# Kernel tuning notes

Measured on AMD Instinct MI355X. Metric: run time of the kernel, lower is better.

Reference implementation:

```python
import jax, jax.numpy as jnp
import numpy as np

K = 9            # LCN box-filter size
EPS = 1e-6


def _box_sum(x):
    """9x9 box sum with zero padding 4, separable. x: [N,H,W] -> [N,H,W]."""
    xp = x[:, None]                                  # N,1,H,W
    kh = jnp.ones((1, 1, K, 1), x.dtype)
    kw = jnp.ones((1, 1, 1, K), x.dtype)
    y = jax.lax.conv_general_dilated(xp, kh, (1, 1), [(K // 2, K // 2), (0, 0)])
    y = jax.lax.conv_general_dilated(y, kw, (1, 1), [(0, 0), (K // 2, K // 2)])
    return y[:, 0]


def _lcn(img):
    """Faithful to torch: conv weight is ones(3,3,9,9)/81, i.e. the 'mean' SUMS over
    the 3 input channels of per-pixel 9x9 box means; every output channel is identical.
    So compute channel-sum once, box-filter it, and broadcast back over channels."""
    kk = float(K * K)
    mean_local = _box_sum(img.sum(axis=1)) / kk                 # N,H,W
    mean_sq_local = _box_sum((img * img).sum(axis=1)) / kk      # N,H,W
    std_local = (mean_sq_local - mean_local * mean_local) * kk / (kk - 1.0)
    m = mean_local[:, None]                                     # N,1,H,W (broadcasts over C)
    s = std_local[:, None]
    return (img - m) / (s + EPS), m, s


def _warp(right, disp):
    """Equivalent of affine_grid(identity) + grid -= (disp*2/W, 0) + grid_sample
    (bilinear, zeros padding, align_corners=False). Since the y-coordinate is the
    identity grid, iy == row index exactly, so sampling reduces to 1-D horizontal
    bilinear interpolation at source column ix = j - disp[n,i,j]."""
    N, C, H, W = right.shape
    ix = jnp.arange(W, dtype=right.dtype)[None, None, :] - disp   # N,H,W
    x0 = jnp.floor(ix)
    wx = ix - x0                                                  # frac weight for x1
    x0i = x0.astype(jnp.int32)
    x1i = x0i + 1
    v0 = ((x0i >= 0) & (x0i < W)).astype(right.dtype)             # zeros padding masks
    v1 = ((x1i >= 0) & (x1i < W)).astype(right.dtype)
    i0 = jnp.broadcast_to(jnp.clip(x0i, 0, W - 1)[:, None], right.shape)
    i1 = jnp.broadcast_to(jnp.clip(x1i, 0, W - 1)[:, None], right.shape)
    g0 = jnp.take_along_axis(right, i0, axis=3)                   # N,C,H,W
    g1 = jnp.take_along_axis(right, i1, axis=3)
    return g0 * (v0 * (1.0 - wx))[:, None] + g1 * (v1 * wx)[:, None]


def setup_inputs() -> dict:
    key = jax.random.key(0)
    k1, k2, k3 = jax.random.split(key, 3)
    N, C, H, W = 8, 3, 720, 1280
    left_img = jax.random.uniform(k1, (N, C, H, W), dtype=jnp.float32)
    right_img = jax.random.uniform(k2, (N, C, H, W), dtype=jnp.float32)
    dispmap = jax.random.uniform(k3, (N, H, W), dtype=jnp.float32) * 64.0  # pixels
    return {"left_img": left_img, "right_img": right_img, "dispmap": dispmap}


def reference(left_img, right_img, dispmap):
    recon_img = _warp(right_img, dispmap)
    recon_img_lcn, _, _ = _lcn(recon_img)
    left_img_lcn, _, left_std_local = _lcn(left_img)
    return jnp.abs((left_img_lcn - recon_img_lcn) * left_std_local).mean()
```

## Files before the change

### kernel.cpp

```cpp
#include <hip/hip_runtime.h>

#define NB 8
#define CC 3
#define HH 720
#define WW 1280
#define EPSL 1e-6f
#define HSEG 15
#define NSEG (HH / HSEG)
#define G4   (NSEG / 4)
#define OUTC 56
#define NSTRIP 23
#define NITER (HSEG + 8)
#define NBLK (NB * NSTRIP * G4)

__device__ __forceinline__ float bperm(int addr, float x) {
    return __int_as_float(__builtin_amdgcn_ds_bpermute(addr, __float_as_int(x)));
}

__global__ __launch_bounds__(256)
void fused_loss_kernel(const float* __restrict__ left,
                       const float* __restrict__ right,
                       const float* __restrict__ disp,
                       float* __restrict__ out)
{
    const int t    = threadIdx.x;
    const int lane = t & 63;
    const int wid  = t >> 6;

    const int b     = blockIdx.x;
    const int strip = b % NSTRIP;
    const int g     = (b / NSTRIP) % G4;
    const int n     = b / (NSTRIP * G4);

    const int h0 = (g * 4 + wid) * HSEG;
    const int gc  = strip * OUTC + lane - 4;
    const int gcc = min(max(gc, 0), WW - 1);
    const float gcf = (float)gc;
    const bool col_ok   = (gc >= 0) && (gc < WW);
    const bool out_lane = (lane >= 4) && (lane < 4 + OUTC) && (gc < WW);

    const size_t plane = (size_t)HH * WW;
    const float* __restrict__ dp  = disp  + (size_t)n * plane;
    const float* __restrict__ lp0 = left  + (size_t)n * CC * plane;
    const float* __restrict__ lp1 = lp0 + plane;
    const float* __restrict__ lp2 = lp1 + plane;
    const float* __restrict__ rp0 = right + (size_t)n * CC * plane;
    const float* __restrict__ rp1 = rp0 + plane;
    const float* __restrict__ rp2 = rp1 + plane;

    const int a_m1 = ((lane + 63) & 63) << 2;
    const int a_p1 = ((lane +  1) & 63) << 2;
    const int a_m3 = ((lane + 61) & 63) << 2;
    const int a_p3 = ((lane +  3) & 63) << 2;

    float4 rg1 = make_float4(0.f,0.f,0.f,0.f);
    float4 rg2=rg1, rg3=rg1, rg4=rg1, rg5=rg1, rg6=rg1, rg7=rg1, rg8=rg1;
    float p1l0=0,p1l1=0,p1l2=0,p1r0=0,p1r1=0,p1r2=0;
    float p2l0=0,p2l1=0,p2l2=0,p2r0=0,p2r1=0,p2r2=0;
    float p3l0=0,p3l1=0,p3l2=0,p3r0=0,p3r1=0,p3r2=0;
    float p4l0=0,p4l1=0,p4l2=0,p4r0=0,p4r1=0,p4r2=0;

    const int r0 = h0 - 4;

    int rcl = min(max(r0, 0), HH - 1);
    unsigned ro = (unsigned)(rcl * WW + gcc);
    float dA  = dp[ro];
    float al0 = lp0[ro], al1 = lp1[ro], al2 = lp2[ro];
    rcl = min(max(r0 + 1, 0), HH - 1);
    unsigned rob = (unsigned)(rcl * WW + gcc);
    float dB  = dp[rob];
    float bl0 = lp0[rob], bl1 = lp1[rob], bl2 = lp2[rob];

    float aw0, aw1, ag00, ag01, ag10, ag11, ag20, ag21;
    {
        float ix  = gcf - dA;
        float x0f = floorf(ix), wx = ix - x0f;
        int x0i = (int)x0f, x1i = x0i + 1;
        float v0 = (x0i >= 0 && x0i < WW) ? 1.f : 0.f;
        float v1 = (x1i >= 0 && x1i < WW) ? 1.f : 0.f;
        int i0 = min(max(x0i, 0), WW - 1), i1 = min(max(x1i, 0), WW - 1);
        aw0 = v0 * (1.f - wx); aw1 = v1 * wx;
        unsigned rb = (unsigned)(min(max(r0, 0), HH - 1) * WW);
        ag00 = rp0[rb + i0]; ag01 = rp0[rb + i1];
        ag10 = rp1[rb + i0]; ag11 = rp1[rb + i1];
        ag20 = rp2[rb + i0]; ag21 = rp2[rb + i1];
    }

    float4 vsum = make_float4(0.f,0.f,0.f,0.f);
    float acc = 0.f;

    for (int iter = 0; iter < NITER; ++iter) {
        const int r = r0 + iter;

        int rcl2 = min(max(r + 2, 0), HH - 1);
        unsigned ro2 = (unsigned)(rcl2 * WW + gcc);
        float dC  = dp[ro2];
        float cl0 = lp0[ro2], cl1 = lp1[ro2], cl2 = lp2[ro2];

        float bw0, bw1, bg00, bg01, bg10, bg11, bg20, bg21;
        {
            float ix  = gcf - dB;
            float x0f = floorf(ix), wx = ix - x0f;
            int x0i = (int)x0f, x1i = x0i + 1;
            float v0 = (x0i >= 0 && x0i < WW) ? 1.f : 0.f;
            float v1 = (x1i >= 0 && x1i < WW) ? 1.f : 0.f;
            int i0 = min(max(x0i, 0), WW - 1), i1 = min(max(x1i, 0), WW - 1);
            bw0 = v0 * (1.f - wx); bw1 = v1 * wx;
            unsigned rb = (unsigned)(min(max(r + 1, 0), HH - 1) * WW);
            bg00 = rp0[rb + i0]; bg01 = rp0[rb + i1];
            bg10 = rp1[rb + i0]; bg11 = rp1[rb + i1];
            bg20 = rp2[rb + i0]; bg21 = rp2[rb + i1];
        }

        float rca = ag00*aw0 + ag01*aw1;
        float rcb = ag10*aw0 + ag11*aw1;
        float rcc = ag20*aw0 + ag21*aw1;
        bool valr = col_ok && ((unsigned)r < (unsigned)HH);
        float rx = al0 + al1 + al2;
        float ry = al0*al0 + al1*al1 + al2*al2;
        float rz = rca + rcb + rcc;
        float rw = rca*rca + rcb*rcb + rcc*rcc;
        rx = valr ? rx : 0.f;  ry = valr ? ry : 0.f;
        rz = valr ? rz : 0.f;  rw = valr ? rw : 0.f;

        float sx = bperm(a_m1, rx) + rx + bperm(a_p1, rx);
        float sy = bperm(a_m1, ry) + ry + bperm(a_p1, ry);
        float sz = bperm(a_m1, rz) + rz + bperm(a_p1, rz);
        float sw = bperm(a_m1, rw) + rw + bperm(a_p1, rw);
        float hx = bperm(a_m3, sx) + sx + bperm(a_p3, sx);
        float hy = bperm(a_m3, sy) + sy + bperm(a_p3, sy);
        float hz = bperm(a_m3, sz) + sz + bperm(a_p3, sz);
        float hw = bperm(a_m3, sw) + sw + bperm(a_p3, sw);

        vsum.x += hx; vsum.y += hy; vsum.z += hz; vsum.w += hw;

        if (iter >= 8) {
            float ml   = vsum.x * (1.f / 81.f);
            float msl  = vsum.y * (1.f / 81.f);
            float stdl = (msl - ml * ml) * (81.f / 80.f);
            float sl   = stdl + EPSL;
            float invl = __builtin_amdgcn_rcpf(sl);
            invl = invl * __builtin_fmaf(-sl, invl, 2.f);
            float mr   = vsum.z * (1.f / 81.f);
            float msr  = vsum.w * (1.f / 81.f);
            float stdr = (msr - mr * mr) * (81.f / 80.f);
            float sr   = stdr + EPSL;
            float invr = __builtin_amdgcn_rcpf(sr);
            invr = invr * __builtin_fmaf(-sr, invr, 2.f);
            if (out_lane) {
                float av, bv;
                av = (p4l0 - ml) * invl; bv = (p4r0 - mr) * invr;
                acc += fabsf((av - bv) * stdl);
                av = (p4l1 - ml) * invl; bv = (p4r1 - mr) * invr;
                acc += fabsf((av - bv) * stdl);
                av = (p4l2 - ml) * invl; bv = (p4r2 - mr) * invr;
                acc += fabsf((av - bv) * stdl);
            }
            vsum.x -= rg8.x; vsum.y -= rg8.y; vsum.z -= rg8.z; vsum.w -= rg8.w;
        }

        rg8 = rg7; rg7 = rg6; rg6 = rg5; rg5 = rg4; rg4 = rg3; rg3 = rg2; rg2 = rg1;
        rg1 = make_float4(hx, hy, hz, hw);
        p4l0=p3l0; p4l1=p3l1; p4l2=p3l2; p4r0=p3r0; p4r1=p3r1; p4r2=p3r2;
        p3l0=p2l0; p3l1=p2l1; p3l2=p2l2; p3r0=p2r0; p3r1=p2r1; p3r2=p2r2;
        p2l0=p1l0; p2l1=p1l1; p2l2=p1l2; p2r0=p1r0; p2r1=p1r1; p2r2=p1r2;
        p1l0=al0;  p1l1=al1;  p1l2=al2;  p1r0=rca;  p1r1=rcb;  p1r2=rcc;

        al0=bl0; al1=bl1; al2=bl2;
        aw0=bw0; aw1=bw1;
        ag00=bg00; ag01=bg01; ag10=bg10; ag11=bg11; ag20=bg20; ag21=bg21;
        dB=dC; bl0=cl0; bl1=cl1; bl2=cl2;
    }

#pragma unroll
    for (int off = 32; off > 0; off >>= 1)
        acc += __shfl_down(acc, off, 64);
    __shared__ float red[4];
    if (lane == 0) red[wid] = acc;
    __syncthreads();
    if (t == 0) {
        float s = red[0] + red[1] + red[2] + red[3];
        const float inv_count = 1.f / ((float)NB * CC * HH * WW);
        atomicAdd(out, s * inv_count);
    }
}

extern "C" void kernel_launch(void* const* d_in, const int* in_sizes, int n_in,
                              void* d_out, int out_size, void* d_ws, size_t ws_size,
                              hipStream_t stream) {
    const float* left  = (const float*)d_in[0];
    const float* right = (const float*)d_in[1];
    const float* disp  = (const float*)d_in[2];
    float* out = (float*)d_out;

    hipMemsetAsync(out, 0, sizeof(float) * out_size, stream);

    hipLaunchKernelGGL(fused_loss_kernel, dim3(NBLK), dim3(256), 0, stream,
                       left, right, disp, out);
}
```

Baseline: 249.2 us.

## Process two batch images per thread and reload left pixels instead of shifting

Each block now handles a pair of images (n and n+4) with interleaved macro-expanded pipelines, so two independent dependency chains run per thread and hide load and bpermute latency. The left-image center values are re-read from global memory (row r-4) instead of being carried through a 4-deep register shift chain. The height segment grows from 15 to 20 rows, which cuts the 8-row halo overhead per output row. In exchange, register pressure roughly doubles, which may lower occupancy, and the block count drops substantially.

```diff
diff --git a/kernel.cpp b/kernel.cpp
--- a/kernel.cpp
+++ b/kernel.cpp
@@ -5,17 +5,127 @@
 #define HH 720
 #define WW 1280
 #define EPSL 1e-6f
-#define HSEG 15
+#define HSEG 20
 #define NSEG (HH / HSEG)
 #define G4   (NSEG / 4)
 #define OUTC 56
 #define NSTRIP 23
 #define NITER (HSEG + 8)
-#define NBLK (NB * NSTRIP * G4)
+#define NPAIR (NB / 2)
+#define NBLK (NPAIR * NSTRIP * G4)
 
 __device__ __forceinline__ float bperm(int addr, float x) {
     return __int_as_float(__builtin_amdgcn_ds_bpermute(addr, __float_as_int(x)));
 }
+
+
+#define DECLS(S) \
+    float4 rg1##S = make_float4(0.f,0.f,0.f,0.f); \
+    float4 rg2##S=rg1##S, rg3##S=rg1##S, rg4##S=rg1##S, rg5##S=rg1##S, \
+           rg6##S=rg1##S, rg7##S=rg1##S, rg8##S=rg1##S; \
+    float q1a##S=0,q1b##S=0,q1c##S=0, q2a##S=0,q2b##S=0,q2c##S=0; \
+    float q3a##S=0,q3b##S=0,q3c##S=0, q4a##S=0,q4b##S=0,q4c##S=0; \
+    float4 vsum##S = make_float4(0.f,0.f,0.f,0.f); \
+    float al##S##0, al##S##1, al##S##2, bl##S##0, bl##S##1, bl##S##2; \
+    float dB##S, aw##S##0, aw##S##1; \
+    float ag##S##00, ag##S##01, ag##S##10, ag##S##11, ag##S##20, ag##S##21;
+
+#define GATH(S, rbase, dv, w0_, w1_, g00_,g01_,g10_,g11_,g20_,g21_) do { \
+    float ix_ = gcf - (dv); float x0f_ = floorf(ix_); float wx_ = ix_ - x0f_; \
+    int x0i_ = (int)x0f_; int x1i_ = x0i_ + 1; \
+    float v0_ = (x0i_ >= 0 && x0i_ < WW) ? 1.f : 0.f; \
+    float v1_ = (x1i_ >= 0 && x1i_ < WW) ? 1.f : 0.f; \
+    int i0_ = min(max(x0i_,0),WW-1); int i1_ = min(max(x1i_,0),WW-1); \
+    w0_ = v0_*(1.f-wx_); w1_ = v1_*wx_; \
+    g00_ = rp##S##0[(rbase)+i0_]; g01_ = rp##S##0[(rbase)+i1_]; \
+    g10_ = rp##S##1[(rbase)+i0_]; g11_ = rp##S##1[(rbase)+i1_]; \
+    g20_ = rp##S##2[(rbase)+i0_]; g21_ = rp##S##2[(rbase)+i1_]; } while(0)
+
+#define PROLOGUE(S) do { \
+    float dA_ = dp##S[oP0]; \
+    al##S##0 = lp##S##0[oP0]; al##S##1 = lp##S##1[oP0]; al##S##2 = lp##S##2[oP0]; \
+    dB##S = dp##S[oP1]; \
+    bl##S##0 = lp##S##0[oP1]; bl##S##1 = lp##S##1[oP1]; bl##S##2 = lp##S##2[oP1]; \
+    GATH(S, rbP, dA_, aw##S##0, aw##S##1, \
+         ag##S##00, ag##S##01, ag##S##10, ag##S##11, ag##S##20, ag##S##21); \
+} while(0)
+
+#define LOADS(S) \
+    float dC##S = dp##S[o2]; \
+    float cl##S##0 = lp##S##0[o2], cl##S##1 = lp##S##1[o2], cl##S##2 = lp##S##2[o2]; \
+    float ol##S##0 = lp##S##0[oo], ol##S##1 = lp##S##1[oo], ol##S##2 = lp##S##2[oo];
+
+#define GATHB(S) \
+    float bw##S##0, bw##S##1; \
+    float bg##S##00, bg##S##01, bg##S##10, bg##S##11, bg##S##20, bg##S##21; \
+    GATH(S, rb1, dB##S, bw##S##0, bw##S##1, \
+         bg##S##00, bg##S##01, bg##S##10, bg##S##11, bg##S##20, bg##S##21);
+
+#define COMBINE(S) \
+    float rca##S = ag##S##00*aw##S##0 + ag##S##01*aw##S##1; \
+    float rcb##S = ag##S##10*aw##S##0 + ag##S##11*aw##S##1; \
+    float rcc##S = ag##S##20*aw##S##0 + ag##S##21*aw##S##1; \
+    float rx##S = al##S##0 + al##S##1 + al##S##2; \
+    float ry##S = al##S##0*al##S##0 + al##S##1*al##S##1 + al##S##2*al##S##2; \
+    float rz##S = rca##S + rcb##S + rcc##S; \
+    float rw##S = rca##S*rca##S + rcb##S*rcb##S + rcc##S*rcc##S; \
+    rx##S = valr ? rx##S : 0.f; ry##S = valr ? ry##S : 0.f; \
+    rz##S = valr ? rz##S : 0.f; rw##S = valr ? rw##S : 0.f;
+
+#define TREE1(S) \
+    float sx##S = bperm(a_m1,rx##S) + rx##S + bperm(a_p1,rx##S); \
+    float sy##S = bperm(a_m1,ry##S) + ry##S + bperm(a_p1,ry##S); \
+    float sz##S = bperm(a_m1,rz##S) + rz##S + bperm(a_p1,rz##S); \
+    float sw##S = bperm(a_m1,rw##S) + rw##S + bperm(a_p1,rw##S);
+
+#define TREE2(S) \
+    float hx##S = bperm(a_m3,sx##S) + sx##S + bperm(a_p3,sx##S); \
+    float hy##S = bperm(a_m3,sy##S) + sy##S + bperm(a_p3,sy##S); \
+    float hz##S = bperm(a_m3,sz##S) + sz##S + bperm(a_p3,sz##S); \
+    float hw##S = bperm(a_m3,sw##S) + sw##S + bperm(a_p3,sw##S);
+
+#define ACCUM(S) \
+    vsum##S.x += hx##S; vsum##S.y += hy##S; vsum##S.z += hz##S; vsum##S.w += hw##S;
+
+#define OUTP(S) do { \
+    float ml_  = vsum##S.x * (1.f/81.f); \
+    float msl_ = vsum##S.y * (1.f/81.f); \
+    float stdl_ = (msl_ - ml_*ml_) * (81.f/80.f); \
+    float sl_ = stdl_ + EPSL; \
+    float invl_ = __builtin_amdgcn_rcpf(sl_); \
+    invl_ = invl_ * __builtin_fmaf(-sl_, invl_, 2.f); \
+    float mr_  = vsum##S.z * (1.f/81.f); \
+    float msr_ = vsum##S.w * (1.f/81.f); \
+    float stdr_ = (msr_ - mr_*mr_) * (81.f/80.f); \
+    float sr_ = stdr_ + EPSL; \
+    float invr_ = __builtin_amdgcn_rcpf(sr_); \
+    invr_ = invr_ * __builtin_fmaf(-sr_, invr_, 2.f); \
+    if (out_lane) { \
+        float av_, bv_; \
+        av_ = (ol##S##0 - ml_)*invl_; bv_ = (q4a##S - mr_)*invr_; \
+        acc += fabsf((av_-bv_)*stdl_); \
+        av_ = (ol##S##1 - ml_)*invl_; bv_ = (q4b##S - mr_)*invr_; \
+        acc += fabsf((av_-bv_)*stdl_); \
+        av_ = (ol##S##2 - ml_)*invl_; bv_ = (q4c##S - mr_)*invr_; \
+        acc += fabsf((av_-bv_)*stdl_); \
+    } \
+    vsum##S.x -= rg8##S.x; vsum##S.y -= rg8##S.y; \
+    vsum##S.z -= rg8##S.z; vsum##S.w -= rg8##S.w; \
+} while(0)
+
+#define SHIFT(S) \
+    rg8##S = rg7##S; rg7##S = rg6##S; rg6##S = rg5##S; rg5##S = rg4##S; \
+    rg4##S = rg3##S; rg3##S = rg2##S; rg2##S = rg1##S; \
+    rg1##S = make_float4(hx##S, hy##S, hz##S, hw##S); \
+    q4a##S=q3a##S; q4b##S=q3b##S; q4c##S=q3c##S; \
+    q3a##S=q2a##S; q3b##S=q2b##S; q3c##S=q2c##S; \
+    q2a##S=q1a##S; q2b##S=q1b##S; q2c##S=q1c##S; \
+    q1a##S=rca##S; q1b##S=rcb##S; q1c##S=rcc##S; \
+    al##S##0=bl##S##0; al##S##1=bl##S##1; al##S##2=bl##S##2; \
+    aw##S##0=bw##S##0; aw##S##1=bw##S##1; \
+    ag##S##00=bg##S##00; ag##S##01=bg##S##01; ag##S##10=bg##S##10; \
+    ag##S##11=bg##S##11; ag##S##20=bg##S##20; ag##S##21=bg##S##21; \
+    dB##S=dC##S; bl##S##0=cl##S##0; bl##S##1=cl##S##1; bl##S##2=cl##S##2;
 
 __global__ __launch_bounds__(256)
 void fused_loss_kernel(const float* __restrict__ left,
@@ -30,7 +140,7 @@
     const int b     = blockIdx.x;
     const int strip = b % NSTRIP;
     const int g     = (b / NSTRIP) % G4;
-    const int n     = b / (NSTRIP * G4);
+    const int np    = b / (NSTRIP * G4);
 
     const int h0 = (g * 4 + wid) * HSEG;
     const int gc  = strip * OUTC + lane - 4;
@@ -40,136 +150,54 @@
     const bool out_lane = (lane >= 4) && (lane < 4 + OUTC) && (gc < WW);
 
     const size_t plane = (size_t)HH * WW;
-    const float* __restrict__ dp  = disp  + (size_t)n * plane;
-    const float* __restrict__ lp0 = left  + (size_t)n * CC * plane;
-    const float* __restrict__ lp1 = lp0 + plane;
-    const float* __restrict__ lp2 = lp1 + plane;
-    const float* __restrict__ rp0 = right + (size_t)n * CC * plane;
-    const float* __restrict__ rp1 = rp0 + plane;
-    const float* __restrict__ rp2 = rp1 + plane;
+    const float* __restrict__ dpA  = disp  + (size_t)np * plane;
+    const float* __restrict__ lpA0 = left  + (size_t)np * CC * plane;
+    const float* __restrict__ lpA1 = lpA0 + plane;
+    const float* __restrict__ lpA2 = lpA1 + plane;
+    const float* __restrict__ rpA0 = right + (size_t)np * CC * plane;
+    const float* __restrict__ rpA1 = rpA0 + plane;
+    const float* __restrict__ rpA2 = rpA1 + plane;
+    const float* __restrict__ dpB  = dpA  + (size_t)NPAIR * plane;
+    const float* __restrict__ lpB0 = lpA0 + (size_t)NPAIR * CC * plane;
+    const float* __restrict__ lpB1 = lpB0 + plane;
+    const float* __restrict__ lpB2 = lpB1 + plane;
+    const float* __restrict__ rpB0 = rpA0 + (size_t)NPAIR * CC * plane;
+    const float* __restrict__ rpB1 = rpB0 + plane;
+    const float* __restrict__ rpB2 = rpB1 + plane;
 
     const int a_m1 = ((lane + 63) & 63) << 2;
     const int a_p1 = ((lane +  1) & 63) << 2;
     const int a_m3 = ((lane + 61) & 63) << 2;
     const int a_p3 = ((lane +  3) & 63) << 2;
 
-    float4 rg1 = make_float4(0.f,0.f,0.f,0.f);
-    float4 rg2=rg1, rg3=rg1, rg4=rg1, rg5=rg1, rg6=rg1, rg7=rg1, rg8=rg1;
-    float p1l0=0,p1l1=0,p1l2=0,p1r0=0,p1r1=0,p1r2=0;
-    float p2l0=0,p2l1=0,p2l2=0,p2r0=0,p2r1=0,p2r2=0;
-    float p3l0=0,p3l1=0,p3l2=0,p3r0=0,p3r1=0,p3r2=0;
-    float p4l0=0,p4l1=0,p4l2=0,p4r0=0,p4r1=0,p4r2=0;
+    DECLS(A)
+    DECLS(B)
 
     const int r0 = h0 - 4;
 
-    int rcl = min(max(r0, 0), HH - 1);
-    unsigned ro = (unsigned)(rcl * WW + gcc);
-    float dA  = dp[ro];
-    float al0 = lp0[ro], al1 = lp1[ro], al2 = lp2[ro];
-    rcl = min(max(r0 + 1, 0), HH - 1);
-    unsigned rob = (unsigned)(rcl * WW + gcc);
-    float dB  = dp[rob];
-    float bl0 = lp0[rob], bl1 = lp1[rob], bl2 = lp2[rob];
-
-    float aw0, aw1, ag00, ag01, ag10, ag11, ag20, ag21;
-    {
-        float ix  = gcf - dA;
-        float x0f = floorf(ix), wx = ix - x0f;
-        int x0i = (int)x0f, x1i = x0i + 1;
-        float v0 = (x0i >= 0 && x0i < WW) ? 1.f : 0.f;
-        float v1 = (x1i >= 0 && x1i < WW) ? 1.f : 0.f;
-        int i0 = min(max(x0i, 0), WW - 1), i1 = min(max(x1i, 0), WW - 1);
-        aw0 = v0 * (1.f - wx); aw1 = v1 * wx;
-        unsigned rb = (unsigned)(min(max(r0, 0), HH - 1) * WW);
-        ag00 = rp0[rb + i0]; ag01 = rp0[rb + i1];
-        ag10 = rp1[rb + i0]; ag11 = rp1[rb + i1];
-        ag20 = rp2[rb + i0]; ag21 = rp2[rb + i1];
-    }
-
-    float4 vsum = make_float4(0.f,0.f,0.f,0.f);
+    const unsigned oP0 = (unsigned)(min(max(r0,     0), HH - 1) * WW) + gcc;
+    const unsigned oP1 = (unsigned)(min(max(r0 + 1, 0), HH - 1) * WW) + gcc;
+    const unsigned rbP = (unsigned)(min(max(r0,     0), HH - 1) * WW);
+    PROLOGUE(A);
+    PROLOGUE(B);
+
     float acc = 0.f;
 
     for (int iter = 0; iter < NITER; ++iter) {
         const int r = r0 + iter;
-
-        int rcl2 = min(max(r + 2, 0), HH - 1);
-        unsigned ro2 = (unsigned)(rcl2 * WW + gcc);
-        float dC  = dp[ro2];
-        float cl0 = lp0[ro2], cl1 = lp1[ro2], cl2 = lp2[ro2];
-
-        float bw0, bw1, bg00, bg01, bg10, bg11, bg20, bg21;
-        {
-            float ix  = gcf - dB;
-            float x0f = floorf(ix), wx = ix - x0f;
-            int x0i = (int)x0f, x1i = x0i + 1;
-            float v0 = (x0i >= 0 && x0i < WW) ? 1.f : 0.f;
-            float v1 = (x1i >= 0 && x1i < WW) ? 1.f : 0.f;
-            int i0 = min(max(x0i, 0), WW - 1), i1 = min(max(x1i, 0), WW - 1);
-            bw0 = v0 * (1.f - wx); bw1 = v1 * wx;
-            unsigned rb = (unsigned)(min(max(r + 1, 0), HH - 1) * WW);
-            bg00 = rp0[rb + i0]; bg01 = rp0[rb + i1];
-            bg10 = rp1[rb + i0]; bg11 = rp1[rb + i1];
-            bg20 = rp2[rb + i0]; bg21 = rp2[rb + i1];
-        }
-
-        float rca = ag00*aw0 + ag01*aw1;
-        float rcb = ag10*aw0 + ag11*aw1;
-        float rcc = ag20*aw0 + ag21*aw1;
-        bool valr = col_ok && ((unsigned)r < (unsigned)HH);
-        float rx = al0 + al1 + al2;
-        float ry = al0*al0 + al1*al1 + al2*al2;
-        float rz = rca + rcb + rcc;
-        float rw = rca*rca + rcb*rcb + rcc*rcc;
-        rx = valr ? rx : 0.f;  ry = valr ? ry : 0.f;
-        rz = valr ? rz : 0.f;  rw = valr ? rw : 0.f;
-
-        float sx = bperm(a_m1, rx) + rx + bperm(a_p1, rx);
-        float sy = bperm(a_m1, ry) + ry + bperm(a_p1, ry);
-        float sz = bperm(a_m1, rz) + rz + bperm(a_p1, rz);
-        float sw = bperm(a_m1, rw) + rw + bperm(a_p1, rw);
-        float hx = bperm(a_m3, sx) + sx + bperm(a_p3, sx);
-        float hy = bperm(a_m3, sy) + sy + bperm(a_p3, sy);
-        float hz = bperm(a_m3, sz) + sz + bperm(a_p3, sz);
-        float hw = bperm(a_m3, sw) + sw + bperm(a_p3, sw);
-
-        vsum.x += hx; vsum.y += hy; vsum.z += hz; vsum.w += hw;
-
-        if (iter >= 8) {
-            float ml   = vsum.x * (1.f / 81.f);
-            float msl  = vsum.y * (1.f / 81.f);
-            float stdl = (msl - ml * ml) * (81.f / 80.f);
-            float sl   = stdl + EPSL;
-            float invl = __builtin_amdgcn_rcpf(sl);
-            invl = invl * __builtin_fmaf(-sl, invl, 2.f);
-            float mr   = vsum.z * (1.f / 81.f);
-            float msr  = vsum.w * (1.f / 81.f);
-            float stdr = (msr - mr * mr) * (81.f / 80.f);
-            float sr   = stdr + EPSL;
-            float invr = __builtin_amdgcn_rcpf(sr);
-            invr = invr * __builtin_fmaf(-sr, invr, 2.f);
-            if (out_lane) {
-                float av, bv;
-                av = (p4l0 - ml) * invl; bv = (p4r0 - mr) * invr;
-                acc += fabsf((av - bv) * stdl);
-                av = (p4l1 - ml) * invl; bv = (p4r1 - mr) * invr;
-                acc += fabsf((av - bv) * stdl);
-                av = (p4l2 - ml) * invl; bv = (p4r2 - mr) * invr;
-                acc += fabsf((av - bv) * stdl);
-            }
-            vsum.x -= rg8.x; vsum.y -= rg8.y; vsum.z -= rg8.z; vsum.w -= rg8.w;
-        }
-
-        rg8 = rg7; rg7 = rg6; rg6 = rg5; rg5 = rg4; rg4 = rg3; rg3 = rg2; rg2 = rg1;
-        rg1 = make_float4(hx, hy, hz, hw);
-        p4l0=p3l0; p4l1=p3l1; p4l2=p3l2; p4r0=p3r0; p4r1=p3r1; p4r2=p3r2;
-        p3l0=p2l0; p3l1=p2l1; p3l2=p2l2; p3r0=p2r0; p3r1=p2r1; p3r2=p2r2;
-        p2l0=p1l0; p2l1=p1l1; p2l2=p1l2; p2r0=p1r0; p2r1=p1r1; p2r2=p1r2;
-        p1l0=al0;  p1l1=al1;  p1l2=al2;  p1r0=rca;  p1r1=rcb;  p1r2=rcc;
-
-        al0=bl0; al1=bl1; al2=bl2;
-        aw0=bw0; aw1=bw1;
-        ag00=bg00; ag01=bg01; ag10=bg10; ag11=bg11; ag20=bg20; ag21=bg21;
-        dB=dC; bl0=cl0; bl1=cl1; bl2=cl2;
+        const unsigned o2  = (unsigned)(min(max(r + 2, 0), HH - 1) * WW) + gcc;
+        const unsigned oo  = (unsigned)(min(max(r - 4, 0), HH - 1) * WW) + gcc;
+        const unsigned rb1 = (unsigned)(min(max(r + 1, 0), HH - 1) * WW);
+        const bool valr = col_ok && ((unsigned)r < (unsigned)HH);
+
+        LOADS(A)  LOADS(B)
+        GATHB(A)  GATHB(B)
+        COMBINE(A) COMBINE(B)
+        TREE1(A)  TREE1(B)
+        TREE2(A)  TREE2(B)
+        ACCUM(A)  ACCUM(B)
+        if (iter >= 8) { OUTP(A); OUTP(B); }
+        SHIFT(A)  SHIFT(B)
     }
 
 #pragma unroll
```

After: 270.8 us. 1.09x slower.
